# Performance work log

Measured on AMD Instinct MI355X. Metric: run time of the kernel, lower is better.

Reference implementation:

```python
import jax, jax.numpy as jnp
import numpy as np

# dims
B, S, T, F = 8, 1024, 32, 64       # batch, stocks(nodes), seq_len, feature
DWV = 64                            # d_word_vec == d_model
RNN = 64                            # GRU hidden (rnn_unit)
NHID = 128                          # n_hid
NH, DK, DV = 4, 16, 16              # heads, d_k, d_v
NC, NE = 2, 128                     # n_class, num hyperedges (H.shape[1])


def setup_inputs() -> dict:
    key = jax.random.key(0)
    ks = jax.random.split(key, 24)
    def p(i, shape):
        return jax.random.normal(ks[i], shape, jnp.float32) / np.float32(np.sqrt(shape[-1]))
    return {
        'src_seq': jax.random.normal(ks[0], (B, S, T, F), jnp.float32),
        'H': jax.random.normal(ks[1], (S, NE), jnp.float32) * 0.1,
        'adj': jax.random.normal(ks[2], (S, S), jnp.float32) * 0.02,
        'n_hid': NHID,
        # GCN (feature -> n_hid -> feature), shared across both adj and H_new branches
        'gcn_W1': p(3, (F, NHID)), 'gcn_b1': jnp.zeros((NHID,), jnp.float32),
        'gcn_W2': p(4, (NHID, F)), 'gcn_b2': jnp.zeros((F,), jnp.float32),
        # Linear(H.shape[1] -> H.shape[0]) created inside forward
        'Wm': p(5, (S, NE)) * 0.1, 'bm': jnp.zeros((S,), jnp.float32),
        # Linear(feature -> d_word_vec)
        'Wl': p(6, (DWV, F)), 'bl': jnp.zeros((DWV,), jnp.float32),
        # 2-layer GRU (batch_first), torch layout W_{ir|iz|in} stacked
        'Wx0': p(7, (3 * RNN, DWV)), 'Wh0': p(8, (3 * RNN, RNN)),
        'bx0': jnp.zeros((3 * RNN,), jnp.float32), 'bh0': jnp.zeros((3 * RNN,), jnp.float32),
        'Wx1': p(9, (3 * RNN, RNN)), 'Wh1': p(10, (3 * RNN, RNN)),
        'bx1': jnp.zeros((3 * RNN,), jnp.float32), 'bh1': jnp.zeros((3 * RNN,), jnp.float32),
        # temporal multi-head attention
        'Wq': p(11, (NH * DK, RNN)), 'Wk': p(12, (NH * DK, RNN)), 'Wv': p(13, (NH * DV, RNN)),
        'Wo': p(14, (RNN, NH * DV)),
        'ln_g': jnp.ones((RNN,), jnp.float32), 'ln_b': jnp.zeros((RNN,), jnp.float32),
        # HGN: two graph-conv layers over stocks, (T*RNN -> n_hid -> n_hid)
        'Wg1': p(15, (T * RNN, NHID)), 'Wg2': p(16, (NHID, NHID)),
        # tgt_word_prj: n_hid -> n_class (no bias)
        'Wp': p(17, (NC, NHID)),
    }


def reference(src_seq, H, adj, n_hid, gcn_W1, gcn_b1, gcn_W2, gcn_b2, Wm, bm,
              Wl, bl, Wx0, Wh0, bx0, bh0, Wx1, Wh1, bx1, bh1,
              Wq, Wk, Wv, Wo, ln_g, ln_b, Wg1, Wg2, Wp):
    b, s, t, f = src_seq.shape

    # per-timestep GCN over the stock (node) axis, fully batched (replaces the
    # double Python loop of mm+spmm in the original)
    def gcn(x, A):  # x: (b,s,t,f), A: (s,s)
        h = jax.nn.relu(jnp.einsum('nm,bmth->bnth', A, x @ gcn_W1) + gcn_b1)
        return jnp.einsum('nm,bmtf->bntf', A, h @ gcn_W2) + gcn_b2

    H_new = H @ Wm.T + bm                       # (s,s) learned hypergraph adjacency
    z = gcn(src_seq, adj) + gcn(src_seq, H_new)  # y_i + y_f for all timesteps

    x = (z @ Wl.T + bl).reshape(b * s, t, -1)    # (N, T, DWV)
    n = b * s

    def gru_layer(xin, Wx, Wh, bx, bh):
        hdim = Wh.shape[1]
        xp = xin @ Wx.T + bx                      # precompute input projections (N,T,3H)
        def step(h, xt):
            gh = h @ Wh.T + bh
            xr, xz, xn = jnp.split(xt, 3, -1)
            hr, hz, hn = jnp.split(gh, 3, -1)
            r = jax.nn.sigmoid(xr + hr)
            zg = jax.nn.sigmoid(xz + hz)
            cand = jnp.tanh(xn + r * hn)
            hnew = (1.0 - zg) * cand + zg * h
            return hnew, hnew
        h0 = jnp.zeros((xin.shape[0], hdim), xin.dtype)
        _, ys = jax.lax.scan(step, h0, jnp.swapaxes(xp, 0, 1))
        return jnp.swapaxes(ys, 0, 1)

    r = gru_layer(gru_layer(x, Wx0, Wh0, bx0, bh0), Wx1, Wh1, bx1, bh1)  # (N,T,RNN)

    # temporal multi-head self-attention with causal (subsequent) mask
    q = (r @ Wq.T).reshape(n, t, NH, DK)
    k = (r @ Wk.T).reshape(n, t, NH, DK)
    v = (r @ Wv.T).reshape(n, t, NH, DV)
    scores = jnp.einsum('nqhd,nkhd->nhqk', q, k) / np.float32(np.sqrt(DK))
    causal = jnp.triu(jnp.ones((t, t), bool), 1)
    attn = jax.nn.softmax(jnp.where(causal, jnp.float32(-1e9), scores), -1)
    o = jnp.einsum('nhqk,nkhd->nqhd', attn, v).reshape(n, t, NH * DV) @ Wo.T + r
    mu = o.mean(-1, keepdims=True)
    o = (o - mu) / jnp.sqrt(o.var(-1, keepdims=True) + 1e-6) * ln_g + ln_b

    enc = o.reshape(b, s, t * o.shape[-1])        # (b, s, T*RNN)

    # HGN: two graph convolutions over the stock axis -> (b, s, n_hid)
    hg = jax.nn.relu(jnp.einsum('nm,bmd->bnd', adj, enc @ Wg1))
    hg = jnp.einsum('nm,bmd->bnd', adj, hg @ Wg2)

    return hg.reshape(b * s, -1) @ Wp.T           # x_logit_scale = 1.0 (no weight sharing)
```

## Files before the change

### kernel.cpp

```cpp
#include <hip/hip_runtime.h>

typedef __attribute__((ext_vector_type(8))) short bf8;
typedef __attribute__((ext_vector_type(4))) float f4;

__device__ __forceinline__ ushort f2b(float f) {
  union { float f; unsigned u; } v; v.f = f;
  unsigned u = v.u + 0x7FFFu + ((v.u >> 16) & 1u);
  return (ushort)(u >> 16);
}
__device__ __forceinline__ float b2f(ushort h) {
  union { unsigned u; float f; } v; v.u = ((unsigned)h) << 16; return v.f;
}
__device__ __forceinline__ bf8 pack8(const float* p) {
  f4 a = *(const f4*)p; f4 b = *(const f4*)(p + 4);
  bf8 t;
  t[0] = (short)f2b(a[0]); t[1] = (short)f2b(a[1]);
  t[2] = (short)f2b(a[2]); t[3] = (short)f2b(a[3]);
  t[4] = (short)f2b(b[0]); t[5] = (short)f2b(b[1]);
  t[6] = (short)f2b(b[2]); t[7] = (short)f2b(b[3]);
  return t;
}
__device__ __forceinline__ float sigm(float x) { return 1.f / (1.f + __expf(-x)); }
__device__ __forceinline__ float tanh_f(float x) {
  float a = fabsf(x), e = __expf(-2.f * a);
  return copysignf((1.f - e) / (1.f + e), x);
}

__device__ __forceinline__ void gl16(const void* g, void* l) {
  __builtin_amdgcn_global_load_lds(
      (const __attribute__((address_space(1))) unsigned int*)(uintptr_t)g,
      (__attribute__((address_space(3))) unsigned int*)(uintptr_t)l, 16, 0, 0);
}

#define SFENCE __builtin_amdgcn_sched_barrier(0)
#define RAWBAR { __builtin_amdgcn_s_barrier(); SFENCE; }
#define WAIT_LGKM0 { asm volatile("s_waitcnt lgkmcnt(0)" ::: "memory"); SFENCE; }
#define WAIT_VM(n) { asm volatile("s_waitcnt vmcnt(" #n ")" ::: "memory"); SFENCE; }

__global__ __launch_bounds__(256) void cvt_k(const float* __restrict__ in,
                                             ushort* __restrict__ out, int n4) {
  int i = blockIdx.x * 256 + threadIdx.x;
  if (i < n4) {
    f4 v = ((const f4*)in)[i];
    ushort4 o;
    o.x = f2b(v[0]); o.y = f2b(v[1]); o.z = f2b(v[2]); o.w = f2b(v[3]);
    ((ushort4*)out)[i] = o;
  }
}

__global__ __launch_bounds__(256) void cvtT_k(const float* __restrict__ in,
                                              ushort* __restrict__ out, int R, int C) {
  __shared__ ushort t[64][68];
  const int tid = threadIdx.x;
  const int r0 = blockIdx.x * 64, c0 = blockIdx.y * 64;
  #pragma unroll
  for (int it = 0; it < 4; ++it) {
    int r = (tid >> 4) + 16 * it, c = (tid & 15) * 4;
    f4 v = *(const f4*)(in + (long)(r0 + r) * C + c0 + c);
    #pragma unroll
    for (int j = 0; j < 4; ++j) t[c + j][r] = f2b(v[j]);
  }
  __syncthreads();
  #pragma unroll
  for (int it = 0; it < 4; ++it) {
    int cc = (tid >> 4) + 16 * it, rr = (tid & 15) * 4;
    ushort4 o = { t[cc][rr], t[cc][rr + 1], t[cc][rr + 2], t[cc][rr + 3] };
    *(ushort4*)(out + (long)(c0 + cc) * R + r0 + rr) = o;
  }
}

__global__ __launch_bounds__(256) void cat_k(const ushort* __restrict__ a,
                                             const ushort* __restrict__ h,
                                             ushort* __restrict__ o) {
  int i = blockIdx.x * 256 + threadIdx.x;
  int s = i >> 7, c8 = (i & 127) << 3;
  *(int4*)(o + (long)s * 2048 + c8) = *(const int4*)(a + (long)s * 1024 + c8);
  *(int4*)(o + (long)s * 2048 + 1024 + c8) = *(const int4*)(h + (long)s * 1024 + c8);
}

__global__ void wcombT_k(const float* __restrict__ Wl, const float* __restrict__ W2,
                         ushort* __restrict__ out) {
  int idx = blockIdx.x * 256 + threadIdx.x;
  int d = idx >> 7, h = idx & 127;
  float s = 0.f;
  #pragma unroll
  for (int f = 0; f < 64; ++f) s += Wl[d * 64 + f] * W2[h * 64 + f];
  out[d * 128 + h] = f2b(s);
}
__global__ void biasc_k(const float* __restrict__ gb2, const float* __restrict__ Wl,
                        const float* __restrict__ bl, float* __restrict__ bc) {
  int d = threadIdx.x;
  float s = 0.f;
  #pragma unroll
  for (int f = 0; f < 64; ++f) s += gb2[f] * Wl[d * 64 + f];
  bc[d] = 2.f * s + bl[d];
}
__global__ void wfin_k(const float* __restrict__ Wg2, const float* __restrict__ Wp,
                       float* __restrict__ wf) {
  int idx = threadIdx.x;
  int d = idx >> 1, c = idx & 1;
  float s = 0.f;
  #pragma unroll
  for (int e = 0; e < 128; ++e) s += Wg2[d * 128 + e] * Wp[c * 128 + e];
  wf[idx] = s;
}

template<int BIASMODE, int RELU, int OUTMODE>
__global__ __launch_bounds__(512, 2) void gemm3_k(
    const ushort* __restrict__ A, const ushort* __restrict__ B,
    ushort* __restrict__ C, const float* __restrict__ bias, int biasMask,
    int N, int K, int lda, int ldb, int ldc,
    long sAq, long sBq, long sCq,
    const ushort* __restrict__ Wc, const float* __restrict__ bcp)
{
  __shared__ __align__(16) ushort As[2 * 256 * 64];
  __shared__ __align__(16) ushort Bs[2 * 256 * 64];
  const int tid = threadIdx.x, lane = tid & 63, wv = tid >> 6;
  const int wm = wv >> 2, wn = wv & 3;
  const long bm = (long)blockIdx.x * 256, bn = (long)blockIdx.y * 256;
  const int z = blockIdx.z;
  const ushort* Ap = A + (long)z * sAq + bm * lda;
  const ushort* Bp = B + (long)z * sBq + bn * ldb;
  ushort* Cp = C + (long)z * sCq;
  const int nt = K >> 6;

  const int srow = wv * 32 + (lane >> 3);
  const int scol = ((lane & 7) ^ (srow & 7)) << 3;
  const ushort* apb = Ap + (long)srow * lda + scol;
  const ushort* bpb = Bp + (long)srow * ldb + scol;

  #define STAGE3(T, D) { \
    const ushort* ap_ = apb + (T) * 64; \
    const ushort* bp_ = bpb + (T) * 64; \
    ushort* la_ = &As[(D) * 16384 + (wv * 32) * 64]; \
    ushort* lb_ = &Bs[(D) * 16384 + (wv * 32) * 64]; \
    _Pragma("unroll") \
    for (int i_ = 0; i_ < 4; ++i_) gl16(ap_ + (long)(i_ * 8) * lda, la_ + i_ * 512); \
    _Pragma("unroll") \
    for (int i_ = 0; i_ < 4; ++i_) gl16(bp_ + (long)(i_ * 8) * ldb, lb_ + i_ * 512); \
  }

  STAGE3(0, 0);
  if (nt > 1) { STAGE3(1, 1); WAIT_VM(8); }
  else        { WAIT_VM(0); }
  RAWBAR;

  f4 acc[8][4] = {};
  for (int t = 0; t < nt; ++t) {
    const int d = t & 1;
    const ushort* as = As + d * 16384;
    const ushort* bs = Bs + d * 16384;
    bf8 b0[4], a0[8];
    #pragma unroll
    for (int n = 0; n < 4; ++n) {
      int r = wn * 64 + n * 16 + (lane & 15);
      b0[n] = *(const bf8*)(bs + r * 64 + (((lane >> 4) ^ (r & 7)) << 3));
    }
    #pragma unroll
    for (int m = 0; m < 8; ++m) {
      int r = wm * 128 + m * 16 + (lane & 15);
      a0[m] = *(const bf8*)(as + r * 64 + (((lane >> 4) ^ (r & 7)) << 3));
    }
    __builtin_amdgcn_s_setprio(1);
    #pragma unroll
    for (int m = 0; m < 8; ++m)
      #pragma unroll
      for (int n = 0; n < 4; ++n)
        acc[m][n] = __builtin_amdgcn_mfma_f32_16x16x32_bf16(a0[m], b0[n], acc[m][n], 0, 0, 0);
    __builtin_amdgcn_s_setprio(0);
    bf8 b1[4], a1[8];
    #pragma unroll
    for (int n = 0; n < 4; ++n) {
      int r = wn * 64 + n * 16 + (lane & 15);
      b1[n] = *(const bf8*)(bs + r * 64 + (((4 + (lane >> 4)) ^ (r & 7)) << 3));
    }
    #pragma unroll
    for (int m = 0; m < 8; ++m) {
      int r = wm * 128 + m * 16 + (lane & 15);
      a1[m] = *(const bf8*)(as + r * 64 + (((4 + (lane >> 4)) ^ (r & 7)) << 3));
    }
    WAIT_LGKM0;
    RAWBAR;
    if (t + 2 < nt) STAGE3(t + 2, d);
    __builtin_amdgcn_s_setprio(1);
    #pragma unroll
    for (int m = 0; m < 8; ++m)
      #pragma unroll
      for (int n = 0; n < 4; ++n)
        acc[m][n] = __builtin_amdgcn_mfma_f32_16x16x32_bf16(a1[m], b1[n], acc[m][n], 0, 0, 0);
    __builtin_amdgcn_s_setprio(0);
    if (t + 1 < nt) {
      if (t + 2 < nt) { WAIT_VM(8); }
      else            { WAIT_VM(0); }
      RAWBAR;
    }
  }
  #undef STAGE3

  if (OUTMODE == 3) {
    ushort* Ps = (wm == 0) ? (ushort*)As : (ushort*)Bs;
    #pragma unroll
    for (int m = 0; m < 8; ++m) {
      int hq = m * 16 + ((lane >> 4) << 2);
      #pragma unroll
      for (int n = 0; n < 4; ++n) {
        int s = wn * 64 + n * 16 + (lane & 15);
        int key = (s & 7) << 4;
        #pragma unroll
        for (int rr = 0; rr < 4; ++rr)
          Ps[s * 128 + ((hq + rr) ^ key)] = f2b(acc[m][n][rr]);
      }
    }
    WAIT_LGKM0;
    RAWBAR;
    const int tl = wm, sq = wn;
    const ushort* Pw = (tl == 0) ? (const ushort*)As : (const ushort*)Bs;
    const int sbase = sq * 64;
    f4 xacc[4][4] = {};
    #pragma unroll
    for (int kk = 0; kk < 4; ++kk) {
      bf8 pa[4], wb[4];
      int hq = kk * 32 + ((lane >> 4) << 3);
      #pragma unroll
      for (int mt = 0; mt < 4; ++mt) {
        int s = sbase + mt * 16 + (lane & 15);
        pa[mt] = *(const bf8*)(Pw + s * 128 + (hq ^ ((s & 7) << 4)));
      }
      #pragma unroll
      for (int ntt = 0; ntt < 4; ++ntt) {
        int dd = ntt * 16 + (lane & 15);
        wb[ntt] = *(const bf8*)(Wc + dd * 128 + hq);
      }
      #pragma unroll
      for (int mt = 0; mt < 4; ++mt)
        #pragma unroll
        for (int ntt = 0; ntt < 4; ++ntt)
          xacc[mt][ntt] = __builtin_amdgcn_mfma_f32_16x16x32_bf16(pa[mt], wb[ntt], xacc[mt][ntt], 0, 0, 0);
    }
    const int tg = (int)(bm >> 7) + tl;
    #pragma unroll
    for (int mt = 0; mt < 4; ++mt)
      #pragma unroll
      for (int ntt = 0; ntt < 4; ++ntt) {
        int dd = ntt * 16 + (lane & 15);
        float bb = bcp[dd];
        #pragma unroll
        for (int rr = 0; rr < 4; ++rr) {
          int s = sbase + mt * 16 + ((lane >> 4) << 2) + rr;
          long seq = (long)z * 1024 + bn + s;
          C[((long)tg * 8192 + seq) * 64 + dd] = f2b(xacc[mt][ntt][rr] + bb);
        }
      }
  } else {
    #pragma unroll
    for (int m = 0; m < 8; ++m) {
      int grow = (int)bm + wm * 128 + m * 16 + ((lane >> 4) << 2);
      #pragma unroll
      for (int n = 0; n < 4; ++n) {
        int col = (int)bn + wn * 64 + n * 16 + (lane & 15);
        #pragma unroll
        for (int rr = 0; rr < 4; ++rr) {
          float v = acc[m][n][rr];
          if (BIASMODE == 1) v += bias[col & biasMask];
          if (BIASMODE == 2) v += bias[(grow + rr) & biasMask];
          if (RELU) v = fmaxf(v, 0.f);
          Cp[(long)(grow + rr) * ldc + col] = f2b(v);
        }
      }
    }
  }
}

template<int BIASMODE, int RELU, int OUTMODE, int SWZ>
__global__ __launch_bounds__(256) void gemm2_k(
    const ushort* __restrict__ A, const ushort* __restrict__ B,
    ushort* __restrict__ C, const float* __restrict__ bias, int biasMask,
    int N, int K, int lda, int ldb, int ldc, int ZD,
    long sAq, long sAr, long sBq, long sBr, long sCq, long sCr)
{
  __shared__ __align__(16) ushort As[2 * 128 * 64];
  __shared__ __align__(16) ushort Bs[2 * 128 * 64];
  const int tid = threadIdx.x, lane = tid & 63, wv = tid >> 6;
  const int wm = wv >> 1, wn = wv & 1;
  int bx = blockIdx.x, by = blockIdx.y;
  const long bm = (long)bx * 128, bn = (long)by * 128;
  int z = blockIdx.z, zq = z, zr = 0;
  if (ZD > 1) { zq = z / ZD; zr = z - zq * ZD; }
  const ushort* Ap = A + (long)zq * sAq + (long)zr * sAr + bm * lda;
  const ushort* Bp = B + (long)zq * sBq + (long)zr * sBr + bn * ldb;
  ushort* Cp = C + (long)zq * sCq + (long)zr * sCr;
  const int nt = K >> 6;

  const int srow = wv * 32 + (lane >> 3);
  const int scol = ((lane & 7) ^ (srow & 7)) << 3;
  const ushort* apb = Ap + (long)srow * lda + scol;
  const ushort* bpb = Bp + (long)srow * ldb + scol;

  #define STAGE(T, D) { \
    const ushort* ap_ = apb + (T) * 64; \
    const ushort* bp_ = bpb + (T) * 64; \
    ushort* la_ = &As[((D) * 128 + wv * 32) * 64]; \
    ushort* lb_ = &Bs[((D) * 128 + wv * 32) * 64]; \
    _Pragma("unroll") \
    for (int i_ = 0; i_ < 4; ++i_) gl16(ap_ + (long)(i_ * 8) * lda, la_ + i_ * 512); \
    _Pragma("unroll") \
    for (int i_ = 0; i_ < 4; ++i_) gl16(bp_ + (long)(i_ * 8) * ldb, lb_ + i_ * 512); \
  }

  STAGE(0, 0);
  if (nt > 1) { STAGE(1, 1); WAIT_VM(8); }
  else        { WAIT_VM(0); }
  RAWBAR;

  f4 acc[4][4] = {};
  for (int t = 0; t < nt; ++t) {
    const int d = t & 1;
    const ushort* as = As + d * 8192;
    const ushort* bs = Bs + d * 8192;
    bf8 af[4][2], bfv[4][2];
    #pragma unroll
    for (int mi = 0; mi < 4; ++mi) {
      int r = wm * 64 + mi * 16 + (lane & 15);
      #pragma unroll
      for (int kk = 0; kk < 2; ++kk) {
        int blk = kk * 4 + (lane >> 4);
        af[mi][kk] = *(const bf8*)(as + r * 64 + ((blk ^ (r & 7)) << 3));
      }
    }
    #pragma unroll
    for (int ni = 0; ni < 4; ++ni) {
      int r = wn * 64 + ni * 16 + (lane & 15);
      #pragma unroll
      for (int kk = 0; kk < 2; ++kk) {
        int blk = kk * 4 + (lane >> 4);
        bfv[ni][kk] = *(const bf8*)(bs + r * 64 + ((blk ^ (r & 7)) << 3));
      }
    }
    WAIT_LGKM0;
    RAWBAR;
    if (t + 2 < nt) STAGE(t + 2, d);
    #pragma unroll
    for (int kk = 0; kk < 2; ++kk)
      #pragma unroll
      for (int mi = 0; mi < 4; ++mi)
        #pragma unroll
        for (int ni = 0; ni < 4; ++ni)
          acc[mi][ni] = __builtin_amdgcn_mfma_f32_16x16x32_bf16(af[mi][kk], bfv[ni][kk], acc[mi][ni], 0, 0, 0);
    if (t + 1 < nt) {
      if (t + 2 < nt) { WAIT_VM(8); }
      else            { WAIT_VM(0); }
      RAWBAR;
    }
  }
  #undef STAGE

  #pragma unroll
  for (int mi = 0; mi < 4; ++mi)
    #pragma unroll
    for (int ni = 0; ni < 4; ++ni) {
      int col = (int)bn + wn * 64 + ni * 16 + (lane & 15);
      if (col < N) {
        if (OUTMODE == 2) {
          int hh = wm * 64 + mi * 16 + (lane >> 4) * 4;
          int tt = (int)(bm >> 7);
          ushort4 o;
          o.x = f2b(acc[mi][ni][0]); o.y = f2b(acc[mi][ni][1]);
          o.z = f2b(acc[mi][ni][2]); o.w = f2b(acc[mi][ni][3]);
          *(ushort4*)(Cp + ((long)col * 32 + tt) * 128 + hh) = o;
        } else {
          #pragma unroll
          for (int rr = 0; rr < 4; ++rr) {
            int row = (int)bm + wm * 64 + mi * 16 + (lane >> 4) * 4 + rr;
            float v = acc[mi][ni][rr];
            if (BIASMODE == 1) v += bias[col & biasMask];
            if (BIASMODE == 2) v += bias[row & biasMask];
            if (RELU) v = fmaxf(v, 0.f);
            Cp[(long)row * ldc + col] = f2b(v);
          }
        }
      }
    }
}

__global__ __launch_bounds__(256) void gemmsk_k(
    const ushort* __restrict__ A, const ushort* __restrict__ B,
    float* __restrict__ P, int Kc, int lda, int ldb,
    long sAq, long sBq)
{
  __shared__ __align__(16) ushort As[2 * 128 * 64];
  __shared__ __align__(16) ushort Bs[2 * 128 * 64];
  const int tid = threadIdx.x, lane = tid & 63, wv = tid >> 6;
  const int wm = wv >> 1, wn = wv & 1;
  const long bm = (long)blockIdx.x * 128, bn = (long)blockIdx.y * 128;
  const int kc = blockIdx.z & 3, zq = blockIdx.z >> 2;
  const ushort* Ap = A + (long)zq * sAq + kc * Kc + bm * lda;
  const ushort* Bp = B + (long)zq * sBq + kc * Kc + bn * ldb;
  const int nt = Kc >> 6;

  const int srow = wv * 32 + (lane >> 3);
  const int scol = ((lane & 7) ^ (srow & 7)) << 3;
  const ushort* apb = Ap + (long)srow * lda + scol;
  const ushort* bpb = Bp + (long)srow * ldb + scol;

  #define STAGEK(T, D) { \
    const ushort* ap_ = apb + (T) * 64; \
    const ushort* bp_ = bpb + (T) * 64; \
    ushort* la_ = &As[((D) * 128 + wv * 32) * 64]; \
    ushort* lb_ = &Bs[((D) * 128 + wv * 32) * 64]; \
    _Pragma("unroll") \
    for (int i_ = 0; i_ < 4; ++i_) gl16(ap_ + (long)(i_ * 8) * lda, la_ + i_ * 512); \
    _Pragma("unroll") \
    for (int i_ = 0; i_ < 4; ++i_) gl16(bp_ + (long)(i_ * 8) * ldb, lb_ + i_ * 512); \
  }

  STAGEK(0, 0);
  if (nt > 1) { STAGEK(1, 1); WAIT_VM(8); }
  else        { WAIT_VM(0); }
  RAWBAR;

  f4 acc[4][4] = {};
  for (int t = 0; t < nt; ++t) {
    const int d = t & 1;
    const ushort* as = As + d * 8192;
    const ushort* bs = Bs + d * 8192;
    bf8 af[4][2], bfv[4][2];
    #pragma unroll
    for (int mi = 0; mi < 4; ++mi) {
      int r = wm * 64 + mi * 16 + (lane & 15);
      #pragma unroll
      for (int kk = 0; kk < 2; ++kk) {
        int blk = kk * 4 + (lane >> 4);
        af[mi][kk] = *(const bf8*)(as + r * 64 + ((blk ^ (r & 7)) << 3));
      }
    }
    #pragma unroll
    for (int ni = 0; ni < 4; ++ni) {
      int r = wn * 64 + ni * 16 + (lane & 15);
      #pragma unroll
      for (int kk = 0; kk < 2; ++kk) {
        int blk = kk * 4 + (lane >> 4);
        bfv[ni][kk] = *(const bf8*)(bs + r * 64 + ((blk ^ (r & 7)) << 3));
      }
    }
    WAIT_LGKM0;
    RAWBAR;
    if (t + 2 < nt) STAGEK(t + 2, d);
    #pragma unroll
    for (int kk = 0; kk < 2; ++kk)
      #pragma unroll
      for (int mi = 0; mi < 4; ++mi)
        #pragma unroll
        for (int ni = 0; ni < 4; ++ni)
          acc[mi][ni] = __builtin_amdgcn_mfma_f32_16x16x32_bf16(af[mi][kk], bfv[ni][kk], acc[mi][ni], 0, 0, 0);
    if (t + 1 < nt) {
      if (t + 2 < nt) { WAIT_VM(8); }
      else            { WAIT_VM(0); }
      RAWBAR;
    }
  }
  #undef STAGEK

  float* Pp = P + (long)blockIdx.z * 131072;
  #pragma unroll
  for (int mi = 0; mi < 4; ++mi)
    #pragma unroll
    for (int ni = 0; ni < 4; ++ni) {
      int col = (int)bn + wn * 64 + ni * 16 + (lane & 15);
      #pragma unroll
      for (int rr = 0; rr < 4; ++rr) {
        int row = (int)bm + wm * 64 + mi * 16 + (lane >> 4) * 4 + rr;
        Pp[(long)row * 1024 + col] = acc[mi][ni][rr];
      }
    }
}

template<int RELU>
__global__ __launch_bounds__(256) void redk_k(const float* __restrict__ P,
                                              ushort* __restrict__ C) {
  int idx = blockIdx.x * 256 + threadIdx.x;
  long z = idx >> 15;
  long rem = (long)(idx & 32767) * 4;
  const float* base = P + z * 4 * 131072 + rem;
  f4 s = *(const f4*)base;
  #pragma unroll
  for (int kc = 1; kc < 4; ++kc) s += *(const f4*)(base + kc * 131072);
  ushort4 o;
  #pragma unroll
  for (int j = 0; j < 4; ++j) {
    float v = s[j];
    if (RELU) v = fmaxf(v, 0.f);
    ((ushort*)&o)[j] = f2b(v);
  }
  *(ushort4*)(C + z * 131072 + rem) = o;
}

__global__ __launch_bounds__(256, 2) void gru_k(
    const ushort* __restrict__ xT,
    const float* __restrict__ Wx0, const float* __restrict__ Wh0,
    const float* __restrict__ bx0, const float* __restrict__ bh0,
    const float* __restrict__ Wx1, const float* __restrict__ Wh1,
    const float* __restrict__ bx1, const float* __restrict__ bh1,
    ushort* __restrict__ rout)
{
  __shared__ ushort hbf[2][2][1024];
  const int tid = threadIdx.x, lane = tid & 63, w = tid >> 6;
  const int seq0 = blockIdx.x * 16;
  for (int i = tid; i < 4096; i += 256) ((ushort*)hbf)[i] = 0;

  const float* Wxp[2] = {Wx0, Wx1};
  const float* Whp[2] = {Wh0, Wh1};
  const float* bxp[2] = {bx0, bx1};
  const float* bhp[2] = {bh0, bh1};
  bf8 Wxf[2][3][2], Whf[2][3][2];
  float bxv[2][3], bhv[2][3];
  #pragma unroll
  for (int L = 0; L < 2; ++L)
    #pragma unroll
    for (int g = 0; g < 3; ++g) {
      int row = g * 64 + w * 16 + (lane & 15);
      bxv[L][g] = bxp[L][row];
      bhv[L][g] = bhp[L][row];
      #pragma unroll
      for (int kk = 0; kk < 2; ++kk) {
        int kb = kk * 32 + (lane >> 4) * 8;
        Wxf[L][g][kk] = pack8(Wxp[L] + row * 64 + kb);
        Whf[L][g][kk] = pack8(Whp[L] + row * 64 + kb);
      }
    }
  __syncthreads();

  const int arow = lane & 15;
  const int col = w * 16 + (lane & 15);
  f4 hprev[2] = {{0.f,0.f,0.f,0.f},{0.f,0.f,0.f,0.f}};
  int pv = 0;
  for (int t = 0; t < 32; ++t) {
    const int cur = pv ^ 1;
    #pragma unroll
    for (int L = 0; L < 2; ++L) {
      bf8 axf[2], ahf[2];
      if (L == 0) {
        const ushort* xb = xT + ((long)t * 8192 + seq0 + arow) * 64 + (lane >> 4) * 8;
        axf[0] = *(const bf8*)(xb);
        axf[1] = *(const bf8*)(xb + 32);
      } else {
        #pragma unroll
        for (int kk = 0; kk < 2; ++kk) {
          int blk = kk * 4 + (lane >> 4);
          axf[kk] = *(const bf8*)(&hbf[0][cur][arow * 64 + ((blk ^ (arow & 7)) << 3)]);
        }
      }
      #pragma unroll
      for (int kk = 0; kk < 2; ++kk) {
        int blk = kk * 4 + (lane >> 4);
        ahf[kk] = *(const bf8*)(&hbf[L][pv][arow * 64 + ((blk ^ (arow & 7)) << 3)]);
      }
      f4 aX[3] = {}; f4 aH[3] = {};
      #pragma unroll
      for (int kk = 0; kk < 2; ++kk)
        #pragma unroll
        for (int g = 0; g < 3; ++g) {
          aX[g] = __builtin_amdgcn_mfma_f32_16x16x32_bf16(axf[kk], Wxf[L][g][kk], aX[g], 0, 0, 0);
          aH[g] = __builtin_amdgcn_mfma_f32_16x16x32_bf16(ahf[kk], Whf[L][g][kk], aH[g], 0, 0, 0);
        }
      f4 hn;
      #pragma unroll
      for (int r = 0; r < 4; ++r) {
        float rg = sigm(aX[0][r] + bxv[L][0] + aH[0][r] + bhv[L][0]);
        float zg = sigm(aX[1][r] + bxv[L][1] + aH[1][r] + bhv[L][1]);
        float cand = tanh_f(aX[2][r] + bxv[L][2] + rg * (aH[2][r] + bhv[L][2]));
        hn[r] = (1.f - zg) * cand + zg * hprev[L][r];
      }
      hprev[L] = hn;
      #pragma unroll
      for (int r = 0; r < 4; ++r) {
        int row = (lane >> 4) * 4 + r;
        ushort hb = f2b(hn[r]);
        hbf[L][cur][row * 64 + (((col >> 3) ^ (row & 7)) << 3) + (col & 7)] = hb;
        if (L == 1) rout[((long)(seq0 + row) * 32 + t) * 64 + col] = hb;
      }
      __syncthreads();
    }
    pv = cur;
  }
}

__global__ __launch_bounds__(256) void attn_k(
    const ushort* __restrict__ r,
    const float* __restrict__ Wq, const float* __restrict__ Wk,
    const float* __restrict__ Wv, const float* __restrict__ Wo,
    const float* __restrict__ lng, const float* __restrict__ lnb,
    ushort* __restrict__ enc)
{
  __shared__ ushort q_s[4][32][40];
  __shared__ ushort k_s[4][32][40];
  __shared__ ushort v_s[4][16][40];
  __shared__ ushort p_s[4][32][40];
  __shared__ ushort o_s[32][88];
  __shared__ float  ln_s[32][68];
  const int tid = threadIdx.x, lane = tid & 63, w = tid >> 6;
  const long n = blockIdx.x;

  for (int i = tid; i < 4 * 32 * 40; i += 256) { ((ushort*)q_s)[i] = 0; ((ushort*)k_s)[i] = 0; }

  bf8 wqf[2], wkf[2], wvf[2], wof[2];
  #pragma unroll
  for (int kk = 0; kk < 2; ++kk) {
    int row = w * 16 + (lane & 15);
    int kb = kk * 32 + (lane >> 4) * 8;
    wqf[kk] = pack8(Wq + row * 64 + kb);
    wkf[kk] = pack8(Wk + row * 64 + kb);
    wvf[kk] = pack8(Wv + row * 64 + kb);
    wof[kk] = pack8(Wo + row * 64 + kb);
  }
  __syncthreads();

  bf8 ar[2][2];
  #pragma unroll
  for (int mi = 0; mi < 2; ++mi)
    #pragma unroll
    for (int kk = 0; kk < 2; ++kk)
      ar[mi][kk] = *(const bf8*)(r + (n * 32 + mi * 16 + (lane & 15)) * 64 + kk * 32 + (lane >> 4) * 8);
  f4 aq[2] = {}, ak[2] = {}, av[2] = {};
  #pragma unroll
  for (int kk = 0; kk < 2; ++kk)
    #pragma unroll
    for (int mi = 0; mi < 2; ++mi) {
      aq[mi] = __builtin_amdgcn_mfma_f32_16x16x32_bf16(ar[mi][kk], wqf[kk], aq[mi], 0, 0, 0);
      ak[mi] = __builtin_amdgcn_mfma_f32_16x16x32_bf16(ar[mi][kk], wkf[kk], ak[mi], 0, 0, 0);
      av[mi] = __builtin_amdgcn_mfma_f32_16x16x32_bf16(ar[mi][kk], wvf[kk], av[mi], 0, 0, 0);
    }
  #pragma unroll
  for (int mi = 0; mi < 2; ++mi)
    #pragma unroll
    for (int rr = 0; rr < 4; ++rr) {
      int row = mi * 16 + (lane >> 4) * 4 + rr;
      q_s[w][row][lane & 15] = f2b(aq[mi][rr]);
      k_s[w][row][lane & 15] = f2b(ak[mi][rr]);
      v_s[w][lane & 15][row] = f2b(av[mi][rr]);
    }

  bf8 a_q[2], b_k[2];
  #pragma unroll
  for (int mt = 0; mt < 2; ++mt)
    a_q[mt] = *(const bf8*)(&q_s[w][mt * 16 + (lane & 15)][(lane >> 4) * 8]);
  #pragma unroll
  for (int nt = 0; nt < 2; ++nt)
    b_k[nt] = *(const bf8*)(&k_s[w][nt * 16 + (lane & 15)][(lane >> 4) * 8]);
  f4 s_[2][2] = {};
  #pragma unroll
  for (int mt = 0; mt < 2; ++mt)
    #pragma unroll
    for (int nt = 0; nt < 2; ++nt)
      s_[mt][nt] = __builtin_amdgcn_mfma_f32_16x16x32_bf16(a_q[mt], b_k[nt], s_[mt][nt], 0, 0, 0);
  #pragma unroll
  for (int mt = 0; mt < 2; ++mt)
    #pragma unroll
    for (int rr = 0; rr < 4; ++rr) {
      int trow = mt * 16 + (lane >> 4) * 4 + rr;
      float s0 = s_[mt][0][rr] * 0.25f, s1 = s_[mt][1][rr] * 0.25f;
      int c0 = lane & 15, c1 = 16 + (lane & 15);
      if (c0 > trow) s0 = -1e30f;
      if (c1 > trow) s1 = -1e30f;
      float m = fmaxf(s0, s1);
      #pragma unroll
      for (int d = 1; d < 16; d <<= 1) m = fmaxf(m, __shfl_xor(m, d));
      float e0 = __expf(s0 - m), e1 = __expf(s1 - m);
      float sum = e0 + e1;
      #pragma unroll
      for (int d = 1; d < 16; d <<= 1) sum += __shfl_xor(sum, d);
      float inv = 1.f / sum;
      p_s[w][trow][c0] = f2b(e0 * inv);
      p_s[w][trow][c1] = f2b(e1 * inv);
    }

  bf8 b_v = *(const bf8*)(&v_s[w][lane & 15][(lane >> 4) * 8]);
  f4 o_[2] = {};
  #pragma unroll
  for (int mt = 0; mt < 2; ++mt) {
    bf8 a_p = *(const bf8*)(&p_s[w][mt * 16 + (lane & 15)][(lane >> 4) * 8]);
    o_[mt] = __builtin_amdgcn_mfma_f32_16x16x32_bf16(a_p, b_v, o_[mt], 0, 0, 0);
  }
  #pragma unroll
  for (int mt = 0; mt < 2; ++mt)
    #pragma unroll
    for (int rr = 0; rr < 4; ++rr)
      o_s[mt * 16 + (lane >> 4) * 4 + rr][w * 16 + (lane & 15)] = f2b(o_[mt][rr]);
  __syncthreads();

  bf8 a_o[2][2];
  #pragma unroll
  for (int mt = 0; mt < 2; ++mt)
    #pragma unroll
    for (int kk = 0; kk < 2; ++kk)
      a_o[mt][kk] = *(const bf8*)(&o_s[mt * 16 + (lane & 15)][kk * 32 + (lane >> 4) * 8]);
  f4 oo[2] = {};
  #pragma unroll
  for (int kk = 0; kk < 2; ++kk)
    #pragma unroll
    for (int mt = 0; mt < 2; ++mt)
      oo[mt] = __builtin_amdgcn_mfma_f32_16x16x32_bf16(a_o[mt][kk], wof[kk], oo[mt], 0, 0, 0);
  #pragma unroll
  for (int mt = 0; mt < 2; ++mt)
    #pragma unroll
    for (int rr = 0; rr < 4; ++rr) {
      int row = mt * 16 + (lane >> 4) * 4 + rr;
      int col = w * 16 + (lane & 15);
      float resid = b2f(r[(n * 32 + row) * 64 + col]);
      ln_s[row][col] = oo[mt][rr] + resid;
    }
  __syncthreads();

  {
    int row = tid >> 3, seg = tid & 7;
    float vals[8], sm = 0.f, sq = 0.f;
    #pragma unroll
    for (int j = 0; j < 8; ++j) {
      float v = ln_s[row][seg * 8 + j];
      vals[j] = v; sm += v; sq += v * v;
    }
    #pragma unroll
    for (int d = 1; d < 8; d <<= 1) { sm += __shfl_xor(sm, d); sq += __shfl_xor(sq, d); }
    float mu = sm * (1.f / 64.f);
    float var = sq * (1.f / 64.f) - mu * mu;
    float rs = rsqrtf(var + 1e-6f);
    union { ushort u[8]; int4 v; } ou;
    #pragma unroll
    for (int j = 0; j < 8; ++j) {
      int c = seg * 8 + j;
      ou.u[j] = f2b((vals[j] - mu) * rs * lng[c] + lnb[c]);
    }
    *(int4*)(enc + (n * 32 + row) * 64 + seg * 8) = ou.v;
  }
}

__global__ __launch_bounds__(256) void final2_k(const ushort* __restrict__ hg3aT,
                                                const float* __restrict__ wf,
                                                float* __restrict__ out) {
  int i = blockIdx.x * 256 + threadIdx.x;
  int b = i >> 10, s = i & 1023;
  const ushort* base = hg3aT + (long)b * 131072 + s;
  float a0 = 0.f, a1 = 0.f;
  #pragma unroll
  for (int d = 0; d < 128; ++d) {
    float v = b2f(base[d * 1024]);
    a0 += v * wf[2 * d];
    a1 += v * wf[2 * d + 1];
  }
  out[2 * i] = a0; out[2 * i + 1] = a1;
}

extern "C" void kernel_launch(void* const* d_in, const int* in_sizes, int n_in,
                              void* d_out, int out_size, void* d_ws, size_t ws_size,
                              hipStream_t stream) {
  const float* src = (const float*)d_in[0];
  const float* H   = (const float*)d_in[1];
  const float* adj = (const float*)d_in[2];
  const float* gW1 = (const float*)d_in[4];
  const float* gb1 = (const float*)d_in[5];
  const float* gW2 = (const float*)d_in[6];
  const float* gb2 = (const float*)d_in[7];
  const float* Wm  = (const float*)d_in[8];
  const float* bm  = (const float*)d_in[9];
  const float* Wl  = (const float*)d_in[10];
  const float* bl  = (const float*)d_in[11];
  const float* Wx0 = (const float*)d_in[12];
  const float* Wh0 = (const float*)d_in[13];
  const float* bx0 = (const float*)d_in[14];
  const float* bh0 = (const float*)d_in[15];
  const float* Wx1 = (const float*)d_in[16];
  const float* Wh1 = (const float*)d_in[17];
  const float* bx1 = (const float*)d_in[18];
  const float* bh1 = (const float*)d_in[19];
  const float* Wq  = (const float*)d_in[20];
  const float* Wk  = (const float*)d_in[21];
  const float* Wv  = (const float*)d_in[22];
  const float* Wo  = (const float*)d_in[23];
  const float* lng = (const float*)d_in[24];
  const float* lnb = (const float*)d_in[25];
  const float* Wg1 = (const float*)d_in[26];
  const float* Wg2 = (const float*)d_in[27];
  const float* Wp  = (const float*)d_in[28];

  char* ws = (char*)d_ws;
  const size_t MB = 1048576ull;
  ushort* adj_bf  = (ushort*)(ws);
  ushort* Hnew_bf = (ushort*)(ws + 2 * MB);
  ushort* H_bf    = (ushort*)(ws + 4 * MB);
  ushort* Wm_bf   = (ushort*)(ws + 4 * MB + 262144);
  ushort* W1T     = (ushort*)(ws + 4 * MB + 524288);
  ushort* WcT     = (ushort*)(ws + 4 * MB + 524288 + 16384);
  float*  bc      = (float*) (ws + 4 * MB + 524288 + 32768);
  float*  wfin    = (float*) (ws + 4 * MB + 524288 + 33792);
  ushort* Wg1T    = (ushort*)(ws + 5 * MB);
  ushort* src_bf  = (ushort*)(ws + 6 * MB);
  ushort* adjcat  = (ushort*)(ws + 6 * MB);
  ushort* XT      = (ushort*)(ws + 38 * MB);
  ushort* xT      = (ushort*)(ws + 38 * MB);
  ushort* r_bf    = (ushort*)(ws + 70 * MB);
  ushort* h1cat   = (ushort*)(ws + 102 * MB);
  ushort* enc     = (ushort*)(ws + 102 * MB);
  float*  Pk      = (float*) (ws + 134 * MB);
  ushort* g1T     = (ushort*)(ws + 150 * MB);
  ushort* hgT     = (ushort*)(ws + 152 * MB);
  ushort* hg3aT   = (ushort*)(ws + 154 * MB);

  auto CVT = [&](const float* in, ushort* out, int n) {
    int n4 = n >> 2;
    cvt_k<<<dim3((n4 + 255) / 256), dim3(256), 0, stream>>>(in, out, n4);
  };
  CVT(src, src_bf, 16777216);
  CVT(adj, adj_bf, 1048576);
  CVT(H, H_bf, 131072);
  CVT(Wm, Wm_bf, 131072);
  cvtT_k<<<dim3(1, 2), 256, 0, stream>>>(gW1, W1T, 64, 128);
  cvtT_k<<<dim3(32, 2), 256, 0, stream>>>(Wg1, Wg1T, 2048, 128);
  wcombT_k<<<dim3(32), 256, 0, stream>>>(Wl, gW2, WcT);
  biasc_k<<<dim3(1), 64, 0, stream>>>(gb2, Wl, bl, bc);
  wfin_k<<<dim3(1), 256, 0, stream>>>(Wg2, Wp, wfin);

  gemm2_k<1,0,0,0><<<dim3(8,8,1),256,0,stream>>>(H_bf, Wm_bf, Hnew_bf, bm, 1023,
      1024, 128, 128, 128, 1024, 1, 0,0, 0,0, 0,0);
  gemm2_k<0,0,0,0><<<dim3(1,8,256),256,0,stream>>>(W1T, src_bf, XT, nullptr, 0,
      1024, 64, 64, 2048, 1024, 32, 0,0, 2097152,64, 4194304,131072);
  cat_k<<<dim3(512),256,0,stream>>>(adj_bf, Hnew_bf, adjcat);
  gemm3_k<2,1,0><<<dim3(16,8,8),512,0,stream>>>(XT, adj_bf, h1cat, gb1, 127,
      2048, 1024, 1024, 1024, 2048, 4194304, 0, 8388608, nullptr, nullptr);
  gemm3_k<0,0,3><<<dim3(16,4,8),512,0,stream>>>(h1cat, adjcat, xT, nullptr, 0,
      1024, 2048, 2048, 2048, 0, 8388608, 0, 0, WcT, bc);
  gru_k<<<dim3(512),dim3(256),0,stream>>>(xT, Wx0,Wh0,bx0,bh0, Wx1,Wh1,bx1,bh1, r_bf);
  attn_k<<<dim3(8192),dim3(256),0,stream>>>(r_bf, Wq,Wk,Wv,Wo, lng,lnb, enc);
  gemmsk_k<<<dim3(1,8,32),256,0,stream>>>(Wg1T, enc, Pk, 512, 2048, 2048, 0, 2097152);
  redk_k<0><<<dim3(1024),256,0,stream>>>(Pk, g1T);
  gemmsk_k<<<dim3(1,8,32),256,0,stream>>>(g1T, adj_bf, Pk, 256, 1024, 1024, 131072, 0);
  redk_k<1><<<dim3(1024),256,0,stream>>>(Pk, hgT);
  gemmsk_k<<<dim3(1,8,32),256,0,stream>>>(hgT, adj_bf, Pk, 256, 1024, 1024, 131072, 0);
  redk_k<0><<<dim3(1024),256,0,stream>>>(Pk, hg3aT);
  final2_k<<<dim3(32),256,0,stream>>>(hg3aT, wfin, (float*)d_out);
}
```

Before: 586.0 us.

## Load GEMM B operand directly from global memory instead of staging through LDS

The B tile is no longer copied into shared memory. Each wave now reads its B fragments straight from global memory into registers every k-step, and only A stays double-buffered in LDS. The prefetch wait counts drop to match the smaller staged traffic, and a separate LDS buffer is kept only for the OUTMODE 3 epilogue. This cuts LDS footprint and LDS traffic for B, but the B loads are unprefetched and issued right before the MFMAs. The waves that share a column block also load the same B data redundantly, and compiler-inserted vmcnt waits may serialize against the A prefetch.

```diff
diff --git a/kernel.cpp b/kernel.cpp
--- a/kernel.cpp
+++ b/kernel.cpp
@@ -114,7 +114,7 @@
     const ushort* __restrict__ Wc, const float* __restrict__ bcp)
 {
   __shared__ __align__(16) ushort As[2 * 256 * 64];
-  __shared__ __align__(16) ushort Bs[2 * 256 * 64];
+  __shared__ __align__(16) ushort Ps2[OUTMODE == 3 ? 32768 : 16];
   const int tid = threadIdx.x, lane = tid & 63, wv = tid >> 6;
   const int wm = wv >> 2, wn = wv & 3;
   const long bm = (long)blockIdx.x * 256, bn = (long)blockIdx.y * 256;
@@ -127,21 +127,17 @@
   const int srow = wv * 32 + (lane >> 3);
   const int scol = ((lane & 7) ^ (srow & 7)) << 3;
   const ushort* apb = Ap + (long)srow * lda + scol;
-  const ushort* bpb = Bp + (long)srow * ldb + scol;
-
-  #define STAGE3(T, D) { \
+  const ushort* bfb = Bp + (long)(wn * 64 + (lane & 15)) * ldb + ((lane >> 4) << 3);
+
+  #define STAGEA(T, D) { \
     const ushort* ap_ = apb + (T) * 64; \
-    const ushort* bp_ = bpb + (T) * 64; \
     ushort* la_ = &As[(D) * 16384 + (wv * 32) * 64]; \
-    ushort* lb_ = &Bs[(D) * 16384 + (wv * 32) * 64]; \
     _Pragma("unroll") \
     for (int i_ = 0; i_ < 4; ++i_) gl16(ap_ + (long)(i_ * 8) * lda, la_ + i_ * 512); \
-    _Pragma("unroll") \
-    for (int i_ = 0; i_ < 4; ++i_) gl16(bp_ + (long)(i_ * 8) * ldb, lb_ + i_ * 512); \
-  }
-
-  STAGE3(0, 0);
-  if (nt > 1) { STAGE3(1, 1); WAIT_VM(8); }
+  }
+
+  STAGEA(0, 0);
+  if (nt > 1) { STAGEA(1, 1); WAIT_VM(4); }
   else        { WAIT_VM(0); }
   RAWBAR;
 
@@ -149,13 +145,10 @@
   for (int t = 0; t < nt; ++t) {
     const int d = t & 1;
     const ushort* as = As + d * 16384;
-    const ushort* bs = Bs + d * 16384;
     bf8 b0[4], a0[8];
     #pragma unroll
-    for (int n = 0; n < 4; ++n) {
-      int r = wn * 64 + n * 16 + (lane & 15);
-      b0[n] = *(const bf8*)(bs + r * 64 + (((lane >> 4) ^ (r & 7)) << 3));
-    }
+    for (int n = 0; n < 4; ++n)
+      b0[n] = *(const bf8*)(bfb + (long)(n * 16) * ldb + t * 64);
     #pragma unroll
     for (int m = 0; m < 8; ++m) {
       int r = wm * 128 + m * 16 + (lane & 15);
@@ -170,10 +163,8 @@
     __builtin_amdgcn_s_setprio(0);
     bf8 b1[4], a1[8];
     #pragma unroll
-    for (int n = 0; n < 4; ++n) {
-      int r = wn * 64 + n * 16 + (lane & 15);
-      b1[n] = *(const bf8*)(bs + r * 64 + (((4 + (lane >> 4)) ^ (r & 7)) << 3));
-    }
+    for (int n = 0; n < 4; ++n)
+      b1[n] = *(const bf8*)(bfb + (long)(n * 16) * ldb + t * 64 + 32);
     #pragma unroll
     for (int m = 0; m < 8; ++m) {
       int r = wm * 128 + m * 16 + (lane & 15);
@@ -181,7 +172,7 @@
     }
     WAIT_LGKM0;
     RAWBAR;
-    if (t + 2 < nt) STAGE3(t + 2, d);
+    if (t + 2 < nt) STAGEA(t + 2, d);
     __builtin_amdgcn_s_setprio(1);
     #pragma unroll
     for (int m = 0; m < 8; ++m)
@@ -190,15 +181,15 @@
         acc[m][n] = __builtin_amdgcn_mfma_f32_16x16x32_bf16(a1[m], b1[n], acc[m][n], 0, 0, 0);
     __builtin_amdgcn_s_setprio(0);
     if (t + 1 < nt) {
-      if (t + 2 < nt) { WAIT_VM(8); }
+      if (t + 2 < nt) { WAIT_VM(4); }
       else            { WAIT_VM(0); }
       RAWBAR;
     }
   }
-  #undef STAGE3
+  #undef STAGEA
 
   if (OUTMODE == 3) {
-    ushort* Ps = (wm == 0) ? (ushort*)As : (ushort*)Bs;
+    ushort* Ps = (wm == 0) ? (ushort*)As : (ushort*)Ps2;
     #pragma unroll
     for (int m = 0; m < 8; ++m) {
       int hq = m * 16 + ((lane >> 4) << 2);
@@ -214,7 +205,7 @@
     WAIT_LGKM0;
     RAWBAR;
     const int tl = wm, sq = wn;
-    const ushort* Pw = (tl == 0) ? (const ushort*)As : (const ushort*)Bs;
+    const ushort* Pw = (tl == 0) ? (const ushort*)As : (const ushort*)Ps2;
     const int sbase = sq * 64;
     f4 xacc[4][4] = {};
     #pragma unroll
```

Result: slower. 727.3 us (+24.1%).
